# Kernel optimization log

Hardware: AMD Instinct MI355X
Metric: run time of the kernel (lower is better)

## Reference

```python
import jax, jax.numpy as jnp
import numpy as np

N, F, T = 128, 32, 5  # nodes, node features, time steps (time_steps=5 in module)
SCALE = 0.1           # scale uniform params so sigmoid/tanh stay non-degenerate


def setup_inputs() -> dict:
    key = jax.random.key(0)
    ks = jax.random.split(key, 10)
    node_features = jax.random.normal(ks[0], (N, F), dtype=jnp.float32)
    A = jax.random.randint(ks[1], (N, N), 0, 9) == 0
    adjacency = (A | A.T) & (~jnp.eye(N, dtype=bool))
    u = lambda k, shape: jax.random.uniform(k, shape, dtype=jnp.float32) * SCALE
    W_u = u(ks[2], (N, N, F, F))   # w_gru_update_gate_features
    U_u = u(ks[3], (N, N, F, F))   # u_gru_update_gate
    W_cm = u(ks[4], (N, N, F, F))  # w_gru_current_memory_message_features
    U_cm = u(ks[5], (N, N, F, F))  # u_gru_current_memory_message
    b_u = u(ks[6], (F,))           # b_gru_update_gate
    b_cm = u(ks[7], (F,))          # b_gru_current_memory_message
    U_nf = u(ks[8], (N, F, F))     # u_graph_node_features
    U_nm = u(ks[9], (N, F, F))     # u_graph_neighbor_messages
    return dict(node_features=node_features, adjacency=adjacency,
                W_u=W_u, U_u=U_u, W_cm=W_cm, U_cm=U_cm,
                b_u=b_u, b_cm=b_cm, U_nf=U_nf, U_nm=U_nm)


def _encode(x, Af, W_u, U_u, W_cm, U_cm, b_u, b_cm, U_nf, U_nm):
    # messages[i, j] = message on directed edge i -> j (edge_slice = (start, end))
    Am = Af[..., None]  # [N, N, 1] edge mask
    # node-feature terms do not depend on messages -> hoist out of the time loop
    Wu_x = jnp.einsum('ijfg,ig->ijf', W_u, x)    # W_u[i,j] @ x[i]
    Wcm_x = jnp.einsum('ijfg,ig->ijf', W_cm, x)  # W_cm[i,j] @ x[i]
    messages = jnp.zeros((N, N, F), dtype=x.dtype)
    for _ in range(T):
        m = messages * Am
        # prev[i,j] = sum_{k in N(i), k != j} messages[k, i]
        S_in = jnp.sum(m, axis=0)                         # [N, F], S_in[i] = sum_k m[k, i]
        prev = S_in[:, None, :] - jnp.swapaxes(m, 0, 1)   # subtract m[j, i]
        # update gate z[i,j] = sigmoid(W_u[i,j]@x_i + U_u[i,j]@prev[i,j] + b_u)
        z = jax.nn.sigmoid(Wu_x + jnp.einsum('ijfg,ijg->ijf', U_u, prev) + b_u)
        # reset gate r[i,k] (same weights as update gate, per source code):
        # r[i,k] = sigmoid(W_u[i,k]@x_i + U_u[i,k]@messages[i,k] + b_u)
        r = jax.nn.sigmoid(Wu_x + jnp.einsum('ijfg,ijg->ijf', U_u, m) + b_u)
        # reset_sum[i,j] = sum_{k in N(i), k != j} r[i,k] * messages[i,k]
        rm = r * m
        reset_sum = jnp.sum(rm, axis=1)[:, None, :] - rm
        # current memory: tanh(W_cm[i,j]@x_i + U_cm[i,j]@reset_sum[i,j] + b_cm)
        cm = jnp.tanh(Wcm_x + jnp.einsum('ijfg,ijg->ijf', U_cm, reset_sum) + b_cm)
        # GRU compose, write only on existing edges (non-edges stay zero)
        messages = ((1.0 - z) * prev + z * cm) * Am
    # node encoding: relu(U_nf[i]@x_i + U_nm[i]@sum_j messages[i, j])
    out_sum = jnp.sum(messages, axis=1)  # [N, F]
    enc = jax.nn.relu(jnp.einsum('ifg,ig->if', U_nf, x) +
                      jnp.einsum('ifg,ig->if', U_nm, out_sum))
    return enc


def reference(node_features, adjacency, W_u, U_u, W_cm, U_cm, b_u, b_cm, U_nf, U_nm):
    Af = adjacency.astype(node_features.dtype)
    return _encode(node_features, Af, W_u, U_u, W_cm, U_cm, b_u, b_cm, U_nf, U_nm)
```

## Files before the change

### kernel.cpp

```cpp
#include <hip/hip_runtime.h>
#include <math.h>

#define NN 128
#define FF 32
#define TT 5

__device__ __forceinline__ float sig_(float v) { return 1.f / (1.f + expf(-v)); }

#define DOT4(acc, u4, vec, g0)                                        \
    acc += u4.x * __shfl(vec, (g0) + 0) + u4.y * __shfl(vec, (g0) + 1) \
         + u4.z * __shfl(vec, (g0) + 2) + u4.w * __shfl(vec, (g0) + 3);

__global__ void k_zero(float* __restrict__ z) {
    z[blockIdx.x * 256 + threadIdx.x] = 0.f;
}

__global__ __launch_bounds__(256) void k_step0(
        const int* __restrict__ adj, const float* __restrict__ x,
        const float* __restrict__ Wu, const float* __restrict__ Wcm,
        const float* __restrict__ Uu,
        const float* __restrict__ bu, const float* __restrict__ bcm,
        float* __restrict__ WUX, float* __restrict__ WCMX,
        float* __restrict__ M1, float* __restrict__ RM,
        float* __restrict__ sin1, float* __restrict__ rout1) {
    const int e = blockIdx.x * 4 + (threadIdx.x >> 6);
    if (!adj[e]) return;
    const int l = threadIdx.x & 63;
    const int i = e >> 7, j = e & 127;
    const int f = l >> 1, h = l & 1, ll = l & 31;
    const float xv = x[i * FF + ll];
    const size_t rb = ((size_t)e * FF + f) * FF + h * 16;
    const float4* __restrict__ wr = (const float4*)(Wu + rb);
    const float4* __restrict__ cr = (const float4*)(Wcm + rb);
    float a0 = 0.f, a1 = 0.f;
#pragma unroll
    for (int q = 0; q < 4; ++q) {
        const float4 w4 = wr[q], c4 = cr[q];
        const int g0 = h * 16 + q * 4;
        DOT4(a0, w4, xv, g0)
        DOT4(a1, c4, xv, g0)
    }
    a0 += __shfl_xor(a0, 1);
    a1 += __shfl_xor(a1, 1);
    const float bu_f = bu[f], bcm_f = bcm[f];
    const float m_pair = sig_(a0 + bu_f) * tanhf(a1 + bcm_f);
    if (h == 0) {
        WUX[(size_t)e * FF + f] = a0;
        WCMX[(size_t)e * FF + f] = a1;
    }
    const float mv = __shfl(m_pair, 2 * ll);
    if (l < 32) {
        M1[(size_t)e * FF + ll] = mv;
        atomicAdd(&sin1[j * FF + ll], mv);
    }
    const float4* __restrict__ ur = (const float4*)(Uu + rb);
    float aR = 0.f;
#pragma unroll
    for (int q = 0; q < 4; ++q) {
        const float4 u4 = ur[q];
        const int g0 = h * 16 + q * 4;
        DOT4(aR, u4, mv, g0)
    }
    aR += __shfl_xor(aR, 1);
    const float rm_pair = sig_(a0 + aR + bu_f) * m_pair;
    const float rmv = __shfl(rm_pair, 2 * ll);
    if (l < 32) {
        RM[(size_t)e * FF + ll] = rmv;
        atomicAdd(&rout1[i * FF + ll], rmv);
    }
}

template <int LAST>
__global__ __launch_bounds__(256) void k_step(
        const int* __restrict__ adj,
        const float* __restrict__ Uu, const float* __restrict__ Ucm,
        const float* __restrict__ bu, const float* __restrict__ bcm,
        const float* __restrict__ WUX, const float* __restrict__ WCMX,
        const float* __restrict__ M_in, float* __restrict__ M_out,
        float* __restrict__ RM,
        const float* __restrict__ sin_t, const float* __restrict__ rout_t,
        float* __restrict__ sin_next, float* __restrict__ rout_next,
        float* __restrict__ outsum) {
    const int e = blockIdx.x * 4 + (threadIdx.x >> 6);
    if (!adj[e]) return;
    const int l = threadIdx.x & 63;
    const int i = e >> 7, j = e & 127;
    const int f = l >> 1, h = l & 1, ll = l & 31;
    const size_t rb = ((size_t)e * FF + f) * FF + h * 16;

    const float prevv = sin_t[i * FF + ll] - M_in[((size_t)j * NN + i) * FF + ll];
    const float4* __restrict__ ur = (const float4*)(Uu + rb);
    const float4 u0 = ur[0], u1 = ur[1], u2 = ur[2], u3 = ur[3];
    float aP = 0.f;
    {
        const int g0 = h * 16;
        DOT4(aP, u0, prevv, g0 + 0)
        DOT4(aP, u1, prevv, g0 + 4)
        DOT4(aP, u2, prevv, g0 + 8)
        DOT4(aP, u3, prevv, g0 + 12)
    }
    aP += __shfl_xor(aP, 1);
    const float bu_f = bu[f];
    const float wux_f = WUX[(size_t)e * FF + f];
    const float z = sig_(wux_f + aP + bu_f);

    const float rsv = rout_t[i * FF + ll] - RM[(size_t)e * FF + ll];
    const float4* __restrict__ crp = (const float4*)(Ucm + rb);
    float aC = 0.f;
    {
        const int g0 = h * 16;
        DOT4(aC, crp[0], rsv, g0 + 0)
        DOT4(aC, crp[1], rsv, g0 + 4)
        DOT4(aC, crp[2], rsv, g0 + 8)
        DOT4(aC, crp[3], rsv, g0 + 12)
    }
    aC += __shfl_xor(aC, 1);
    const float cmv = tanhf(WCMX[(size_t)e * FF + f] + aC + bcm[f]);

    const float prev_f = __shfl(prevv, f);
    const float m_pair = (1.f - z) * prev_f + z * cmv;
    const float mv = __shfl(m_pair, 2 * ll);

    if (LAST) {
        if (l < 32) atomicAdd(&outsum[i * FF + ll], mv);
    } else {
        if (l < 32) {
            M_out[(size_t)e * FF + ll] = mv;
            atomicAdd(&sin_next[j * FF + ll], mv);
        }
        float aR = 0.f;
        {
            const int g0 = h * 16;
            DOT4(aR, u0, mv, g0 + 0)
            DOT4(aR, u1, mv, g0 + 4)
            DOT4(aR, u2, mv, g0 + 8)
            DOT4(aR, u3, mv, g0 + 12)
        }
        aR += __shfl_xor(aR, 1);
        const float rm_pair = sig_(wux_f + aR + bu_f) * m_pair;
        const float rmv = __shfl(rm_pair, 2 * ll);
        if (l < 32) {
            RM[(size_t)e * FF + ll] = rmv;
            atomicAdd(&rout_next[i * FF + ll], rmv);
        }
    }
}

__global__ void k_final(const float* __restrict__ x, const float* __restrict__ outsum,
                        const float* __restrict__ Unf, const float* __restrict__ Unm,
                        float* __restrict__ out) {
    const int i = blockIdx.x;
    const int l = threadIdx.x;
    const int f = l >> 1, h = l & 1, ll = l & 31;
    const float xv = x[i * FF + ll];
    const float ov = outsum[i * FF + ll];
    const size_t rb = ((size_t)i * FF + f) * FF + h * 16;
    const float4* __restrict__ fr = (const float4*)(Unf + rb);
    const float4* __restrict__ mr = (const float4*)(Unm + rb);
    float a = 0.f;
#pragma unroll
    for (int q = 0; q < 4; ++q) {
        const float4 f4 = fr[q], m4 = mr[q];
        const int g0 = h * 16 + q * 4;
        DOT4(a, f4, xv, g0)
        DOT4(a, m4, ov, g0)
    }
    a += __shfl_xor(a, 1);
    if (h == 0) out[i * FF + f] = fmaxf(a, 0.f);
}

extern "C" void kernel_launch(void* const* d_in, const int* in_sizes, int n_in,
                              void* d_out, int out_size, void* d_ws, size_t ws_size,
                              hipStream_t stream) {
    const float* x   = (const float*)d_in[0];
    const int*   adj = (const int*)d_in[1];
    const float* Wu  = (const float*)d_in[2];
    const float* Uu  = (const float*)d_in[3];
    const float* Wcm = (const float*)d_in[4];
    const float* Ucm = (const float*)d_in[5];
    const float* bu  = (const float*)d_in[6];
    const float* bcm = (const float*)d_in[7];
    const float* Unf = (const float*)d_in[8];
    const float* Unm = (const float*)d_in[9];
    float* out = (float*)d_out;

    const size_t EF = (size_t)NN * NN * FF;
    const size_t NF = (size_t)NN * FF;
    float* p    = (float*)d_ws;
    float* MA   = p; p += EF;
    float* MB   = p; p += EF;
    float* WUX  = p; p += EF;
    float* WCMX = p; p += EF;
    float* RM   = p; p += EF;
    float* acc  = p; p += 9 * NF;
    float* sinb[4]  = {acc, acc + NF, acc + 2 * NF, acc + 3 * NF};
    float* routb[4] = {acc + 4 * NF, acc + 5 * NF, acc + 6 * NF, acc + 7 * NF};
    float* outsum   = acc + 8 * NF;

    const int EG = (NN * NN) / 4;

    k_zero<<<(9 * NF) / 256, 256, 0, stream>>>(acc);
    k_step0<<<EG, 256, 0, stream>>>(adj, x, Wu, Wcm, Uu, bu, bcm,
                                    WUX, WCMX, MA, RM, sinb[0], routb[0]);
    k_step<0><<<EG, 256, 0, stream>>>(adj, Uu, Ucm, bu, bcm, WUX, WCMX,
                                      MA, MB, RM, sinb[0], routb[0],
                                      sinb[1], routb[1], outsum);
    k_step<0><<<EG, 256, 0, stream>>>(adj, Uu, Ucm, bu, bcm, WUX, WCMX,
                                      MB, MA, RM, sinb[1], routb[1],
                                      sinb[2], routb[2], outsum);
    k_step<0><<<EG, 256, 0, stream>>>(adj, Uu, Ucm, bu, bcm, WUX, WCMX,
                                      MA, MB, RM, sinb[2], routb[2],
                                      sinb[3], routb[3], outsum);
    k_step<1><<<EG, 256, 0, stream>>>(adj, Uu, Ucm, bu, bcm, WUX, WCMX,
                                      MB, MA, RM, sinb[3], routb[3],
                                      nullptr, nullptr, outsum);
    k_final<<<NN, 64, 0, stream>>>(x, outsum, Unf, Unm, out);
}
```

Baseline: 46.47 us.

## Fuse last GRU step with final encoding and replace shuffles with vector loads

After: 63.55 us. 36.8% more time.

```diff
diff --git a/kernel.cpp b/kernel.cpp
--- a/kernel.cpp
+++ b/kernel.cpp
@@ -3,13 +3,28 @@
 
 #define NN 128
 #define FF 32
-#define TT 5
+#define DCAP 64
 
 __device__ __forceinline__ float sig_(float v) { return 1.f / (1.f + expf(-v)); }
 
-#define DOT4(acc, u4, vec, g0)                                        \
-    acc += u4.x * __shfl(vec, (g0) + 0) + u4.y * __shfl(vec, (g0) + 1) \
-         + u4.z * __shfl(vec, (g0) + 2) + u4.w * __shfl(vec, (g0) + 3);
+__device__ __forceinline__ void ld16(float* __restrict__ d, const float* s) {
+    const float4* p = (const float4*)s;
+    const float4 a = p[0], b = p[1], c = p[2], e4 = p[3];
+    d[0]=a.x;  d[1]=a.y;  d[2]=a.z;  d[3]=a.w;
+    d[4]=b.x;  d[5]=b.y;  d[6]=b.z;  d[7]=b.w;
+    d[8]=c.x;  d[9]=c.y;  d[10]=c.z; d[11]=c.w;
+    d[12]=e4.x; d[13]=e4.y; d[14]=e4.z; d[15]=e4.w;
+}
+
+__device__ __forceinline__ float dot16(const float4 a, const float4 b,
+                                       const float4 c, const float4 d,
+                                       const float* __restrict__ w) {
+    float s = a.x*w[0] + a.y*w[1] + a.z*w[2] + a.w*w[3];
+    s += b.x*w[4] + b.y*w[5] + b.z*w[6] + b.w*w[7];
+    s += c.x*w[8] + c.y*w[9] + c.z*w[10] + c.w*w[11];
+    s += d.x*w[12] + d.y*w[13] + d.z*w[14] + d.w*w[15];
+    return s;
+}
 
 __global__ void k_zero(float* __restrict__ z) {
     z[blockIdx.x * 256 + threadIdx.x] = 0.f;
@@ -23,54 +38,48 @@
         float* __restrict__ WUX, float* __restrict__ WCMX,
         float* __restrict__ M1, float* __restrict__ RM,
         float* __restrict__ sin1, float* __restrict__ rout1) {
-    const int e = blockIdx.x * 4 + (threadIdx.x >> 6);
+    __shared__ float lm[4][FF], lrm[4][FF];
+    const int wv = threadIdx.x >> 6;
+    const int e = blockIdx.x * 4 + wv;
     if (!adj[e]) return;
     const int l = threadIdx.x & 63;
     const int i = e >> 7, j = e & 127;
     const int f = l >> 1, h = l & 1, ll = l & 31;
-    const float xv = x[i * FF + ll];
-    const size_t rb = ((size_t)e * FF + f) * FF + h * 16;
-    const float4* __restrict__ wr = (const float4*)(Wu + rb);
-    const float4* __restrict__ cr = (const float4*)(Wcm + rb);
-    float a0 = 0.f, a1 = 0.f;
-#pragma unroll
-    for (int q = 0; q < 4; ++q) {
-        const float4 w4 = wr[q], c4 = cr[q];
-        const int g0 = h * 16 + q * 4;
-        DOT4(a0, w4, xv, g0)
-        DOT4(a1, c4, xv, g0)
-    }
+    const int w0 = h * 16;
+    const size_t rb = ((size_t)e * FF + f) * FF + w0;
+
+    float xw[16];
+    ld16(xw, x + i * FF + w0);
+    const float4* wp = (const float4*)(Wu + rb);
+    float a0 = dot16(wp[0], wp[1], wp[2], wp[3], xw);
     a0 += __shfl_xor(a0, 1);
+    const float4* cp = (const float4*)(Wcm + rb);
+    float a1 = dot16(cp[0], cp[1], cp[2], cp[3], xw);
     a1 += __shfl_xor(a1, 1);
-    const float bu_f = bu[f], bcm_f = bcm[f];
-    const float m_pair = sig_(a0 + bu_f) * tanhf(a1 + bcm_f);
+    const float bu_f = bu[f];
     if (h == 0) {
         WUX[(size_t)e * FF + f] = a0;
         WCMX[(size_t)e * FF + f] = a1;
     }
-    const float mv = __shfl(m_pair, 2 * ll);
+    const float mn = sig_(a0 + bu_f) * tanhf(a1 + bcm[f]);
+    if (h == 0) lm[wv][f] = mn;
+    float vw[16];
+    ld16(vw, &lm[wv][w0]);
+    const float4* up = (const float4*)(Uu + rb);
+    float aR = dot16(up[0], up[1], up[2], up[3], vw);
+    aR += __shfl_xor(aR, 1);
+    const float rp = sig_(a0 + aR + bu_f);
+    if (h == 0) lrm[wv][f] = rp * mn;
     if (l < 32) {
-        M1[(size_t)e * FF + ll] = mv;
-        atomicAdd(&sin1[j * FF + ll], mv);
-    }
-    const float4* __restrict__ ur = (const float4*)(Uu + rb);
-    float aR = 0.f;
-#pragma unroll
-    for (int q = 0; q < 4; ++q) {
-        const float4 u4 = ur[q];
-        const int g0 = h * 16 + q * 4;
-        DOT4(aR, u4, mv, g0)
-    }
-    aR += __shfl_xor(aR, 1);
-    const float rm_pair = sig_(a0 + aR + bu_f) * m_pair;
-    const float rmv = __shfl(rm_pair, 2 * ll);
-    if (l < 32) {
+        const float mvv = lm[wv][ll];
+        M1[(size_t)e * FF + ll] = mvv;
+        atomicAdd(&sin1[j * FF + ll], mvv);
+        const float rmv = lrm[wv][ll];
         RM[(size_t)e * FF + ll] = rmv;
         atomicAdd(&rout1[i * FF + ll], rmv);
     }
 }
 
-template <int LAST>
 __global__ __launch_bounds__(256) void k_step(
         const int* __restrict__ adj,
         const float* __restrict__ Uu, const float* __restrict__ Ucm,
@@ -79,94 +88,142 @@
         const float* __restrict__ M_in, float* __restrict__ M_out,
         float* __restrict__ RM,
         const float* __restrict__ sin_t, const float* __restrict__ rout_t,
-        float* __restrict__ sin_next, float* __restrict__ rout_next,
-        float* __restrict__ outsum) {
-    const int e = blockIdx.x * 4 + (threadIdx.x >> 6);
+        float* __restrict__ sin_next, float* __restrict__ rout_next) {
+    __shared__ float lm[4][FF], lrm[4][FF];
+    const int wv = threadIdx.x >> 6;
+    const int e = blockIdx.x * 4 + wv;
     if (!adj[e]) return;
     const int l = threadIdx.x & 63;
     const int i = e >> 7, j = e & 127;
     const int f = l >> 1, h = l & 1, ll = l & 31;
-    const size_t rb = ((size_t)e * FF + f) * FF + h * 16;
-
-    const float prevv = sin_t[i * FF + ll] - M_in[((size_t)j * NN + i) * FF + ll];
-    const float4* __restrict__ ur = (const float4*)(Uu + rb);
-    const float4 u0 = ur[0], u1 = ur[1], u2 = ur[2], u3 = ur[3];
-    float aP = 0.f;
-    {
-        const int g0 = h * 16;
-        DOT4(aP, u0, prevv, g0 + 0)
-        DOT4(aP, u1, prevv, g0 + 4)
-        DOT4(aP, u2, prevv, g0 + 8)
-        DOT4(aP, u3, prevv, g0 + 12)
-    }
+    const int w0 = h * 16;
+    const size_t rb = ((size_t)e * FF + f) * FF + w0;
+
+    const float4* up = (const float4*)(Uu + rb);
+    const float4 u0 = up[0], u1 = up[1], u2 = up[2], u3 = up[3];
+
+    float sw[16], mw[16], vw[16];
+    ld16(sw, sin_t + i * FF + w0);
+    ld16(mw, M_in + ((size_t)j * NN + i) * FF + w0);
+#pragma unroll
+    for (int k = 0; k < 16; ++k) vw[k] = sw[k] - mw[k];
+    float aP = dot16(u0, u1, u2, u3, vw);
     aP += __shfl_xor(aP, 1);
-    const float bu_f = bu[f];
+    const float bu_f  = bu[f];
     const float wux_f = WUX[(size_t)e * FF + f];
     const float z = sig_(wux_f + aP + bu_f);
 
-    const float rsv = rout_t[i * FF + ll] - RM[(size_t)e * FF + ll];
-    const float4* __restrict__ crp = (const float4*)(Ucm + rb);
-    float aC = 0.f;
-    {
-        const int g0 = h * 16;
-        DOT4(aC, crp[0], rsv, g0 + 0)
-        DOT4(aC, crp[1], rsv, g0 + 4)
-        DOT4(aC, crp[2], rsv, g0 + 8)
-        DOT4(aC, crp[3], rsv, g0 + 12)
-    }
+    ld16(sw, rout_t + i * FF + w0);
+    ld16(mw, RM + (size_t)e * FF + w0);
+#pragma unroll
+    for (int k = 0; k < 16; ++k) vw[k] = sw[k] - mw[k];
+    const float4* cp = (const float4*)(Ucm + rb);
+    float aC = dot16(cp[0], cp[1], cp[2], cp[3], vw);
     aC += __shfl_xor(aC, 1);
     const float cmv = tanhf(WCMX[(size_t)e * FF + f] + aC + bcm[f]);
 
-    const float prev_f = __shfl(prevv, f);
-    const float m_pair = (1.f - z) * prev_f + z * cmv;
-    const float mv = __shfl(m_pair, 2 * ll);
-
-    if (LAST) {
-        if (l < 32) atomicAdd(&outsum[i * FF + ll], mv);
-    } else {
-        if (l < 32) {
-            M_out[(size_t)e * FF + ll] = mv;
-            atomicAdd(&sin_next[j * FF + ll], mv);
-        }
-        float aR = 0.f;
-        {
-            const int g0 = h * 16;
-            DOT4(aR, u0, mv, g0 + 0)
-            DOT4(aR, u1, mv, g0 + 4)
-            DOT4(aR, u2, mv, g0 + 8)
-            DOT4(aR, u3, mv, g0 + 12)
-        }
-        aR += __shfl_xor(aR, 1);
-        const float rm_pair = sig_(wux_f + aR + bu_f) * m_pair;
-        const float rmv = __shfl(rm_pair, 2 * ll);
-        if (l < 32) {
-            RM[(size_t)e * FF + ll] = rmv;
-            atomicAdd(&rout_next[i * FF + ll], rmv);
-        }
-    }
-}
-
-__global__ void k_final(const float* __restrict__ x, const float* __restrict__ outsum,
-                        const float* __restrict__ Unf, const float* __restrict__ Unm,
-                        float* __restrict__ out) {
+    const float prev_f = sin_t[i * FF + f] - M_in[((size_t)j * NN + i) * FF + f];
+    const float mn = (1.f - z) * prev_f + z * cmv;
+    if (h == 0) lm[wv][f] = mn;
+    ld16(vw, &lm[wv][w0]);
+    float aR = dot16(u0, u1, u2, u3, vw);
+    aR += __shfl_xor(aR, 1);
+    const float rp = sig_(wux_f + aR + bu_f);
+    if (h == 0) lrm[wv][f] = rp * mn;
+    if (l < 32) {
+        const float mvv = lm[wv][ll];
+        M_out[(size_t)e * FF + ll] = mvv;
+        atomicAdd(&sin_next[j * FF + ll], mvv);
+        const float rmv = lrm[wv][ll];
+        RM[(size_t)e * FF + ll] = rmv;
+        atomicAdd(&rout_next[i * FF + ll], rmv);
+    }
+}
+
+__global__ __launch_bounds__(512) void k_last(
+        const int* __restrict__ adj, const float* __restrict__ x,
+        const float* __restrict__ Uu, const float* __restrict__ Ucm,
+        const float* __restrict__ bu, const float* __restrict__ bcm,
+        const float* __restrict__ WUX, const float* __restrict__ WCMX,
+        const float* __restrict__ M_in, const float* __restrict__ RM,
+        const float* __restrict__ sin4, const float* __restrict__ rout4,
+        const float* __restrict__ Unf, const float* __restrict__ Unm,
+        float* __restrict__ out) {
     const int i = blockIdx.x;
-    const int l = threadIdx.x;
-    const int f = l >> 1, h = l & 1, ll = l & 31;
-    const float xv = x[i * FF + ll];
-    const float ov = outsum[i * FF + ll];
-    const size_t rb = ((size_t)i * FF + f) * FF + h * 16;
-    const float4* __restrict__ fr = (const float4*)(Unf + rb);
-    const float4* __restrict__ mr = (const float4*)(Unm + rb);
-    float a = 0.f;
-#pragma unroll
-    for (int q = 0; q < 4; ++q) {
-        const float4 f4 = fr[q], m4 = mr[q];
-        const int g0 = h * 16 + q * 4;
-        DOT4(a, f4, xv, g0)
-        DOT4(a, m4, ov, g0)
-    }
-    a += __shfl_xor(a, 1);
-    if (h == 0) out[i * FF + f] = fmaxf(a, 0.f);
+    const int t = threadIdx.x;
+    const int wv = t >> 6, l = t & 63;
+    const int f = l >> 1, h = l & 1;
+    const int w0 = h * 16;
+
+    __shared__ int nbr[DCAP];
+    __shared__ int wcnt[2];
+    __shared__ float sin_s[FF], rout_s[FF], xs[FF], os_s[FF];
+    __shared__ float opp[8][FF];
+
+    const bool pred = (t < NN) && (adj[i * NN + t] != 0);
+    const unsigned long long mask = __ballot(pred);
+    if (wv < 2 && l == 0) wcnt[wv] = __popcll(mask);
+    if (t < FF) {
+        sin_s[t]  = sin4[i * FF + t];
+        rout_s[t] = rout4[i * FF + t];
+        xs[t]     = x[i * FF + t];
+    }
+    __syncthreads();
+    if (pred) {
+        const int base = (wv == 1) ? wcnt[0] : 0;
+        nbr[base + __popcll(mask & ((1ull << (unsigned)l) - 1ull))] = t;
+    }
+    __syncthreads();
+    const int dg = wcnt[0] + wcnt[1];
+
+    float osf = 0.f;
+    for (int s = wv; s < dg; s += 8) {
+        const int j = nbr[s];
+        const size_t e = (size_t)i * NN + j;
+        const size_t rb = (e * FF + f) * FF + w0;
+        float sw[16], mw[16], vw[16];
+        ld16(sw, &sin_s[w0]);
+        ld16(mw, M_in + ((size_t)j * NN + i) * FF + w0);
+#pragma unroll
+        for (int k = 0; k < 16; ++k) vw[k] = sw[k] - mw[k];
+        const float4* up = (const float4*)(Uu + rb);
+        float aP = dot16(up[0], up[1], up[2], up[3], vw);
+        aP += __shfl_xor(aP, 1);
+        const float z = sig_(WUX[e * FF + f] + aP + bu[f]);
+
+        ld16(sw, &rout_s[w0]);
+        ld16(mw, RM + e * FF + w0);
+#pragma unroll
+        for (int k = 0; k < 16; ++k) vw[k] = sw[k] - mw[k];
+        const float4* cp = (const float4*)(Ucm + rb);
+        float aC = dot16(cp[0], cp[1], cp[2], cp[3], vw);
+        aC += __shfl_xor(aC, 1);
+        const float cmv = tanhf(WCMX[e * FF + f] + aC + bcm[f]);
+
+        const float prev_f = sin_s[f] - M_in[((size_t)j * NN + i) * FF + f];
+        osf += (1.f - z) * prev_f + z * cmv;
+    }
+    if (h == 0) opp[wv][f] = osf;
+    __syncthreads();
+    if (t < FF) {
+        float s = 0.f;
+#pragma unroll
+        for (int g = 0; g < 8; ++g) s += opp[g][t];
+        os_s[t] = s;
+    }
+    __syncthreads();
+    if (t < 64) {
+        const size_t rb = ((size_t)i * FF + f) * FF + w0;
+        float xw[16], ow[16];
+        ld16(xw, &xs[w0]);
+        ld16(ow, &os_s[w0]);
+        const float4* fp = (const float4*)(Unf + rb);
+        const float4* mp = (const float4*)(Unm + rb);
+        float a = dot16(fp[0], fp[1], fp[2], fp[3], xw)
+                + dot16(mp[0], mp[1], mp[2], mp[3], ow);
+        a += __shfl_xor(a, 1);
+        if (h == 0) out[i * FF + f] = fmaxf(a, 0.f);
+    }
 }
 
 extern "C" void kernel_launch(void* const* d_in, const int* in_sizes, int n_in,
@@ -192,27 +249,24 @@
     float* WUX  = p; p += EF;
     float* WCMX = p; p += EF;
     float* RM   = p; p += EF;
-    float* acc  = p; p += 9 * NF;
+    float* acc  = p; p += 8 * NF;
     float* sinb[4]  = {acc, acc + NF, acc + 2 * NF, acc + 3 * NF};
     float* routb[4] = {acc + 4 * NF, acc + 5 * NF, acc + 6 * NF, acc + 7 * NF};
-    float* outsum   = acc + 8 * NF;
 
     const int EG = (NN * NN) / 4;
 
-    k_zero<<<(9 * NF) / 256, 256, 0, stream>>>(acc);
+    k_zero<<<(8 * NF) / 256, 256, 0, stream>>>(acc);
     k_step0<<<EG, 256, 0, stream>>>(adj, x, Wu, Wcm, Uu, bu, bcm,
                                     WUX, WCMX, MA, RM, sinb[0], routb[0]);
-    k_step<0><<<EG, 256, 0, stream>>>(adj, Uu, Ucm, bu, bcm, WUX, WCMX,
-                                      MA, MB, RM, sinb[0], routb[0],
-                                      sinb[1], routb[1], outsum);
-    k_step<0><<<EG, 256, 0, stream>>>(adj, Uu, Ucm, bu, bcm, WUX, WCMX,
-                                      MB, MA, RM, sinb[1], routb[1],
-                                      sinb[2], routb[2], outsum);
-    k_step<0><<<EG, 256, 0, stream>>>(adj, Uu, Ucm, bu, bcm, WUX, WCMX,
-                                      MA, MB, RM, sinb[2], routb[2],
-                                      sinb[3], routb[3], outsum);
-    k_step<1><<<EG, 256, 0, stream>>>(adj, Uu, Ucm, bu, bcm, WUX, WCMX,
-                                      MB, MA, RM, sinb[3], routb[3],
-                                      nullptr, nullptr, outsum);
-    k_final<<<NN, 64, 0, stream>>>(x, outsum, Unf, Unm, out);
-}
+    k_step<<<EG, 256, 0, stream>>>(adj, Uu, Ucm, bu, bcm, WUX, WCMX,
+                                   MA, MB, RM, sinb[0], routb[0],
+                                   sinb[1], routb[1]);
+    k_step<<<EG, 256, 0, stream>>>(adj, Uu, Ucm, bu, bcm, WUX, WCMX,
+                                   MB, MA, RM, sinb[1], routb[1],
+                                   sinb[2], routb[2]);
+    k_step<<<EG, 256, 0, stream>>>(adj, Uu, Ucm, bu, bcm, WUX, WCMX,
+                                   MA, MB, RM, sinb[2], routb[2],
+                                   sinb[3], routb[3]);
+    k_last<<<NN, 512, 0, stream>>>(adj, x, Uu, Ucm, bu, bcm, WUX, WCMX,
+                                   MB, RM, sinb[3], routb[3], Unf, Unm, out);
+}
```

## Compact edge list and fuse last GRU step with node output

Applied to the files above, without the earlier changes.

After: 50.14 us. +7.9%, slower.

```diff
diff --git a/kernel.cpp b/kernel.cpp
--- a/kernel.cpp
+++ b/kernel.cpp
@@ -3,127 +3,170 @@
 
 #define NN 128
 #define FF 32
-#define TT 5
+#define NBLK_E 896
+#define GSTRIDE (NBLK_E * 4)
 
 __device__ __forceinline__ float sig_(float v) { return 1.f / (1.f + expf(-v)); }
 
-#define DOT4(acc, u4, vec, g0)                                        \
+#define DOT4(acc, u4, vec, g0)                                         \
     acc += u4.x * __shfl(vec, (g0) + 0) + u4.y * __shfl(vec, (g0) + 1) \
          + u4.z * __shfl(vec, (g0) + 2) + u4.w * __shfl(vec, (g0) + 3);
 
-__global__ void k_zero(float* __restrict__ z) {
-    z[blockIdx.x * 256 + threadIdx.x] = 0.f;
+__global__ __launch_bounds__(1024) void k_prep(
+        const int* __restrict__ adj, float* __restrict__ acc,
+        int* __restrict__ elist, int* __restrict__ meta) {
+    const int t = threadIdx.x, lane = t & 63, wid = t >> 6;
+    for (int g = t; g < 8 * NN * FF; g += 1024) acc[g] = 0.f;
+
+    const int4* ap = (const int4*)(adj + t * 16);
+    const int4 v0 = ap[0], v1 = ap[1], v2 = ap[2], v3 = ap[3];
+    const int c[16] = {v0.x, v0.y, v0.z, v0.w, v1.x, v1.y, v1.z, v1.w,
+                       v2.x, v2.y, v2.z, v2.w, v3.x, v3.y, v3.z, v3.w};
+    int fl = 0;
+#pragma unroll
+    for (int k = 0; k < 16; ++k)
+        if (c[k]) fl |= (1 << k);
+    const int cnt = __popc(fl);
+
+    int inc = cnt;
+#pragma unroll
+    for (int d = 1; d < 64; d <<= 1) {
+        const int n = __shfl_up(inc, d);
+        if (lane >= d) inc += n;
+    }
+    __shared__ int wtot[16], wbase[16], Etot_s;
+    if (lane == 63) wtot[wid] = inc;
+    __syncthreads();
+    if (t < 16) {
+        const int v = wtot[t];
+        int pz = v;
+#pragma unroll
+        for (int d = 1; d < 16; d <<= 1) {
+            const int n = __shfl_up(pz, d);
+            if (t >= d) pz += n;
+        }
+        wbase[t] = pz - v;
+        if (t == 15) Etot_s = pz;
+    }
+    __syncthreads();
+    const int base = wbase[wid] + (inc - cnt);
+    if ((t & 7) == 0) meta[1 + (t >> 3)] = base;
+    if (t == 0) { meta[0] = Etot_s; meta[129] = Etot_s; }
+    int off = base;
+#pragma unroll
+    for (int k = 0; k < 16; ++k)
+        if ((fl >> k) & 1) elist[off++] = t * 16 + k;
 }
 
 __global__ __launch_bounds__(256) void k_step0(
-        const int* __restrict__ adj, const float* __restrict__ x,
+        const int* __restrict__ elist, const int* __restrict__ meta,
+        const float* __restrict__ x,
         const float* __restrict__ Wu, const float* __restrict__ Wcm,
         const float* __restrict__ Uu,
         const float* __restrict__ bu, const float* __restrict__ bcm,
         float* __restrict__ WUX, float* __restrict__ WCMX,
         float* __restrict__ M1, float* __restrict__ RM,
         float* __restrict__ sin1, float* __restrict__ rout1) {
-    const int e = blockIdx.x * 4 + (threadIdx.x >> 6);
-    if (!adj[e]) return;
+    const int E = meta[0];
+    const int gw = blockIdx.x * 4 + (threadIdx.x >> 6);
     const int l = threadIdx.x & 63;
-    const int i = e >> 7, j = e & 127;
     const int f = l >> 1, h = l & 1, ll = l & 31;
-    const float xv = x[i * FF + ll];
-    const size_t rb = ((size_t)e * FF + f) * FF + h * 16;
-    const float4* __restrict__ wr = (const float4*)(Wu + rb);
-    const float4* __restrict__ cr = (const float4*)(Wcm + rb);
-    float a0 = 0.f, a1 = 0.f;
-#pragma unroll
-    for (int q = 0; q < 4; ++q) {
-        const float4 w4 = wr[q], c4 = cr[q];
-        const int g0 = h * 16 + q * 4;
-        DOT4(a0, w4, xv, g0)
-        DOT4(a1, c4, xv, g0)
-    }
-    a0 += __shfl_xor(a0, 1);
-    a1 += __shfl_xor(a1, 1);
     const float bu_f = bu[f], bcm_f = bcm[f];
-    const float m_pair = sig_(a0 + bu_f) * tanhf(a1 + bcm_f);
-    if (h == 0) {
-        WUX[(size_t)e * FF + f] = a0;
-        WCMX[(size_t)e * FF + f] = a1;
-    }
-    const float mv = __shfl(m_pair, 2 * ll);
-    if (l < 32) {
-        M1[(size_t)e * FF + ll] = mv;
-        atomicAdd(&sin1[j * FF + ll], mv);
-    }
-    const float4* __restrict__ ur = (const float4*)(Uu + rb);
-    float aR = 0.f;
-#pragma unroll
-    for (int q = 0; q < 4; ++q) {
-        const float4 u4 = ur[q];
-        const int g0 = h * 16 + q * 4;
-        DOT4(aR, u4, mv, g0)
-    }
-    aR += __shfl_xor(aR, 1);
-    const float rm_pair = sig_(a0 + aR + bu_f) * m_pair;
-    const float rmv = __shfl(rm_pair, 2 * ll);
-    if (l < 32) {
-        RM[(size_t)e * FF + ll] = rmv;
-        atomicAdd(&rout1[i * FF + ll], rmv);
-    }
-}
-
-template <int LAST>
+    for (int slot = gw; slot < E; slot += GSTRIDE) {
+        const int e = elist[slot];
+        const int i = e >> 7, j = e & 127;
+        const size_t rb = ((size_t)e * FF + f) * FF + h * 16;
+        const float xv = x[i * FF + ll];
+        const float4* __restrict__ wp = (const float4*)(Wu + rb);
+        const float4* __restrict__ cp = (const float4*)(Wcm + rb);
+        float a0 = 0.f, a1 = 0.f;
+#pragma unroll
+        for (int q = 0; q < 4; ++q) {
+            const float4 w4 = wp[q], c4 = cp[q];
+            const int g0 = h * 16 + q * 4;
+            DOT4(a0, w4, xv, g0)
+            DOT4(a1, c4, xv, g0)
+        }
+        a0 += __shfl_xor(a0, 1);
+        a1 += __shfl_xor(a1, 1);
+        if (h == 0) {
+            WUX[(size_t)e * FF + f] = a0;
+            WCMX[(size_t)e * FF + f] = a1;
+        }
+        const float m_pair = sig_(a0 + bu_f) * tanhf(a1 + bcm_f);
+        const float mv = __shfl(m_pair, 2 * ll);
+        if (l < 32) {
+            M1[(size_t)e * FF + ll] = mv;
+            atomicAdd(&sin1[j * FF + ll], mv);
+        }
+        const float4* __restrict__ up = (const float4*)(Uu + rb);
+        float aR = 0.f;
+#pragma unroll
+        for (int q = 0; q < 4; ++q) {
+            const float4 u4 = up[q];
+            const int g0 = h * 16 + q * 4;
+            DOT4(aR, u4, mv, g0)
+        }
+        aR += __shfl_xor(aR, 1);
+        const float rm_pair = sig_(a0 + aR + bu_f) * m_pair;
+        const float rmv = __shfl(rm_pair, 2 * ll);
+        if (l < 32) {
+            RM[(size_t)e * FF + ll] = rmv;
+            atomicAdd(&rout1[i * FF + ll], rmv);
+        }
+    }
+}
+
 __global__ __launch_bounds__(256) void k_step(
-        const int* __restrict__ adj,
+        const int* __restrict__ elist, const int* __restrict__ meta,
         const float* __restrict__ Uu, const float* __restrict__ Ucm,
         const float* __restrict__ bu, const float* __restrict__ bcm,
         const float* __restrict__ WUX, const float* __restrict__ WCMX,
         const float* __restrict__ M_in, float* __restrict__ M_out,
         float* __restrict__ RM,
         const float* __restrict__ sin_t, const float* __restrict__ rout_t,
-        float* __restrict__ sin_next, float* __restrict__ rout_next,
-        float* __restrict__ outsum) {
-    const int e = blockIdx.x * 4 + (threadIdx.x >> 6);
-    if (!adj[e]) return;
+        float* __restrict__ sin_next, float* __restrict__ rout_next) {
+    const int E = meta[0];
+    const int gw = blockIdx.x * 4 + (threadIdx.x >> 6);
     const int l = threadIdx.x & 63;
-    const int i = e >> 7, j = e & 127;
     const int f = l >> 1, h = l & 1, ll = l & 31;
-    const size_t rb = ((size_t)e * FF + f) * FF + h * 16;
-
-    const float prevv = sin_t[i * FF + ll] - M_in[((size_t)j * NN + i) * FF + ll];
-    const float4* __restrict__ ur = (const float4*)(Uu + rb);
-    const float4 u0 = ur[0], u1 = ur[1], u2 = ur[2], u3 = ur[3];
-    float aP = 0.f;
-    {
-        const int g0 = h * 16;
-        DOT4(aP, u0, prevv, g0 + 0)
-        DOT4(aP, u1, prevv, g0 + 4)
-        DOT4(aP, u2, prevv, g0 + 8)
-        DOT4(aP, u3, prevv, g0 + 12)
-    }
-    aP += __shfl_xor(aP, 1);
-    const float bu_f = bu[f];
-    const float wux_f = WUX[(size_t)e * FF + f];
-    const float z = sig_(wux_f + aP + bu_f);
-
-    const float rsv = rout_t[i * FF + ll] - RM[(size_t)e * FF + ll];
-    const float4* __restrict__ crp = (const float4*)(Ucm + rb);
-    float aC = 0.f;
-    {
-        const int g0 = h * 16;
-        DOT4(aC, crp[0], rsv, g0 + 0)
-        DOT4(aC, crp[1], rsv, g0 + 4)
-        DOT4(aC, crp[2], rsv, g0 + 8)
-        DOT4(aC, crp[3], rsv, g0 + 12)
-    }
-    aC += __shfl_xor(aC, 1);
-    const float cmv = tanhf(WCMX[(size_t)e * FF + f] + aC + bcm[f]);
-
-    const float prev_f = __shfl(prevv, f);
-    const float m_pair = (1.f - z) * prev_f + z * cmv;
-    const float mv = __shfl(m_pair, 2 * ll);
-
-    if (LAST) {
-        if (l < 32) atomicAdd(&outsum[i * FF + ll], mv);
-    } else {
+    const float bu_f = bu[f], bcm_f = bcm[f];
+    for (int slot = gw; slot < E; slot += GSTRIDE) {
+        const int e = elist[slot];
+        const int i = e >> 7, j = e & 127;
+        const size_t rb = ((size_t)e * FF + f) * FF + h * 16;
+
+        const float prevv = sin_t[i * FF + ll] - M_in[((size_t)j * NN + i) * FF + ll];
+        const float4* __restrict__ up = (const float4*)(Uu + rb);
+        const float4 u0 = up[0], u1 = up[1], u2 = up[2], u3 = up[3];
+        float aP = 0.f;
+        {
+            const int g0 = h * 16;
+            DOT4(aP, u0, prevv, g0 + 0)
+            DOT4(aP, u1, prevv, g0 + 4)
+            DOT4(aP, u2, prevv, g0 + 8)
+            DOT4(aP, u3, prevv, g0 + 12)
+        }
+        aP += __shfl_xor(aP, 1);
+        const float wux_f = WUX[(size_t)e * FF + f];
+        const float z = sig_(wux_f + aP + bu_f);
+
+        const float rsv = rout_t[i * FF + ll] - RM[(size_t)e * FF + ll];
+        const float4* __restrict__ cp = (const float4*)(Ucm + rb);
+        float aC = 0.f;
+        {
+            const int g0 = h * 16;
+            DOT4(aC, cp[0], rsv, g0 + 0)
+            DOT4(aC, cp[1], rsv, g0 + 4)
+            DOT4(aC, cp[2], rsv, g0 + 8)
+            DOT4(aC, cp[3], rsv, g0 + 12)
+        }
+        aC += __shfl_xor(aC, 1);
+        const float cmv = tanhf(WCMX[(size_t)e * FF + f] + aC + bcm_f);
+
+        const float prev_f = __shfl(prevv, f);
+        const float m_pair = (1.f - z) * prev_f + z * cmv;
+        const float mv = __shfl(m_pair, 2 * ll);
         if (l < 32) {
             M_out[(size_t)e * FF + ll] = mv;
             atomicAdd(&sin_next[j * FF + ll], mv);
@@ -146,27 +189,82 @@
     }
 }
 
-__global__ void k_final(const float* __restrict__ x, const float* __restrict__ outsum,
-                        const float* __restrict__ Unf, const float* __restrict__ Unm,
-                        float* __restrict__ out) {
+__global__ __launch_bounds__(1024) void k_last(
+        const int* __restrict__ elist, const int* __restrict__ meta,
+        const float* __restrict__ x,
+        const float* __restrict__ Uu, const float* __restrict__ Ucm,
+        const float* __restrict__ bu, const float* __restrict__ bcm,
+        const float* __restrict__ WUX, const float* __restrict__ WCMX,
+        const float* __restrict__ M_in, const float* __restrict__ RM,
+        const float* __restrict__ sin4, const float* __restrict__ rout4,
+        const float* __restrict__ Unf, const float* __restrict__ Unm,
+        float* __restrict__ out) {
     const int i = blockIdx.x;
-    const int l = threadIdx.x;
+    const int t = threadIdx.x;
+    const int wv = t >> 6, l = t & 63;
     const int f = l >> 1, h = l & 1, ll = l & 31;
-    const float xv = x[i * FF + ll];
-    const float ov = outsum[i * FF + ll];
-    const size_t rb = ((size_t)i * FF + f) * FF + h * 16;
-    const float4* __restrict__ fr = (const float4*)(Unf + rb);
-    const float4* __restrict__ mr = (const float4*)(Unm + rb);
-    float a = 0.f;
-#pragma unroll
-    for (int q = 0; q < 4; ++q) {
-        const float4 f4 = fr[q], m4 = mr[q];
-        const int g0 = h * 16 + q * 4;
-        DOT4(a, f4, xv, g0)
-        DOT4(a, m4, ov, g0)
-    }
-    a += __shfl_xor(a, 1);
-    if (h == 0) out[i * FF + f] = fmaxf(a, 0.f);
+    const int rs = meta[1 + i], re = meta[2 + i];
+    const float sinv = sin4[i * FF + ll];
+    const float routv = rout4[i * FF + ll];
+    const float bu_f = bu[f], bcm_f = bcm[f];
+
+    float osv = 0.f;
+    for (int s = rs + wv; s < re; s += 16) {
+        const int e = elist[s];
+        const int j = e & 127;
+        const size_t rb = ((size_t)e * FF + f) * FF + h * 16;
+        const float prevv = sinv - M_in[((size_t)j * NN + i) * FF + ll];
+        const float4* __restrict__ up = (const float4*)(Uu + rb);
+        float aP = 0.f;
+        {
+            const int g0 = h * 16;
+            DOT4(aP, up[0], prevv, g0 + 0)
+            DOT4(aP, up[1], prevv, g0 + 4)
+            DOT4(aP, up[2], prevv, g0 + 8)
+            DOT4(aP, up[3], prevv, g0 + 12)
+        }
+        aP += __shfl_xor(aP, 1);
+        const float z = sig_(WUX[(size_t)e * FF + f] + aP + bu_f);
+
+        const float rsv = routv - RM[(size_t)e * FF + ll];
+        const float4* __restrict__ cp = (const float4*)(Ucm + rb);
+        float aC = 0.f;
+        {
+            const int g0 = h * 16;
+            DOT4(aC, cp[0], rsv, g0 + 0)
+            DOT4(aC, cp[1], rsv, g0 + 4)
+            DOT4(aC, cp[2], rsv, g0 + 8)
+            DOT4(aC, cp[3], rsv, g0 + 12)
+        }
+        aC += __shfl_xor(aC, 1);
+        const float cmv = tanhf(WCMX[(size_t)e * FF + f] + aC + bcm_f);
+
+        const float prev_f = __shfl(prevv, f);
+        const float m_pair = (1.f - z) * prev_f + z * cmv;
+        osv += __shfl(m_pair, 2 * ll);
+    }
+    __shared__ float opp[16][FF];
+    if (l < 32) opp[wv][ll] = osv;
+    __syncthreads();
+    if (t < 64) {
+        float os = 0.f;
+#pragma unroll
+        for (int g = 0; g < 16; ++g) os += opp[g][ll];
+        const float xv = x[i * FF + ll];
+        const size_t rb = ((size_t)i * FF + f) * FF + h * 16;
+        const float4* __restrict__ fp = (const float4*)(Unf + rb);
+        const float4* __restrict__ mp = (const float4*)(Unm + rb);
+        float a = 0.f;
+#pragma unroll
+        for (int q = 0; q < 4; ++q) {
+            const float4 f4 = fp[q], m4 = mp[q];
+            const int g0 = h * 16 + q * 4;
+            DOT4(a, f4, xv, g0)
+            DOT4(a, m4, os, g0)
+        }
+        a += __shfl_xor(a, 1);
+        if (h == 0) out[i * FF + f] = fmaxf(a, 0.f);
+    }
 }
 
 extern "C" void kernel_launch(void* const* d_in, const int* in_sizes, int n_in,
@@ -192,27 +290,25 @@
     float* WUX  = p; p += EF;
     float* WCMX = p; p += EF;
     float* RM   = p; p += EF;
-    float* acc  = p; p += 9 * NF;
+    float* acc  = p; p += 8 * NF;
+    int* elist  = (int*)p;
+    int* meta   = elist + NN * NN;
     float* sinb[4]  = {acc, acc + NF, acc + 2 * NF, acc + 3 * NF};
     float* routb[4] = {acc + 4 * NF, acc + 5 * NF, acc + 6 * NF, acc + 7 * NF};
-    float* outsum   = acc + 8 * NF;
-
-    const int EG = (NN * NN) / 4;
-
-    k_zero<<<(9 * NF) / 256, 256, 0, stream>>>(acc);
-    k_step0<<<EG, 256, 0, stream>>>(adj, x, Wu, Wcm, Uu, bu, bcm,
-                                    WUX, WCMX, MA, RM, sinb[0], routb[0]);
-    k_step<0><<<EG, 256, 0, stream>>>(adj, Uu, Ucm, bu, bcm, WUX, WCMX,
-                                      MA, MB, RM, sinb[0], routb[0],
-                                      sinb[1], routb[1], outsum);
-    k_step<0><<<EG, 256, 0, stream>>>(adj, Uu, Ucm, bu, bcm, WUX, WCMX,
-                                      MB, MA, RM, sinb[1], routb[1],
-                                      sinb[2], routb[2], outsum);
-    k_step<0><<<EG, 256, 0, stream>>>(adj, Uu, Ucm, bu, bcm, WUX, WCMX,
-                                      MA, MB, RM, sinb[2], routb[2],
-                                      sinb[3], routb[3], outsum);
-    k_step<1><<<EG, 256, 0, stream>>>(adj, Uu, Ucm, bu, bcm, WUX, WCMX,
-                                      MB, MA, RM, sinb[3], routb[3],
-                                      nullptr, nullptr, outsum);
-    k_final<<<NN, 64, 0, stream>>>(x, outsum, Unf, Unm, out);
-}
+
+    k_prep<<<1, 1024, 0, stream>>>(adj, acc, elist, meta);
+    k_step0<<<NBLK_E, 256, 0, stream>>>(elist, meta, x, Wu, Wcm, Uu, bu, bcm,
+                                        WUX, WCMX, MA, RM, sinb[0], routb[0]);
+    k_step<<<NBLK_E, 256, 0, stream>>>(elist, meta, Uu, Ucm, bu, bcm, WUX, WCMX,
+                                       MA, MB, RM, sinb[0], routb[0],
+                                       sinb[1], routb[1]);
+    k_step<<<NBLK_E, 256, 0, stream>>>(elist, meta, Uu, Ucm, bu, bcm, WUX, WCMX,
+                                       MB, MA, RM, sinb[1], routb[1],
+                                       sinb[2], routb[2]);
+    k_step<<<NBLK_E, 256, 0, stream>>>(elist, meta, Uu, Ucm, bu, bcm, WUX, WCMX,
+                                       MA, MB, RM, sinb[2], routb[2],
+                                       sinb[3], routb[3]);
+    k_last<<<NN, 1024, 0, stream>>>(elist, meta, x, Uu, Ucm, bu, bcm,
+                                    WUX, WCMX, MB, RM, sinb[3], routb[3],
+                                    Unf, Unm, out);
+}
```
